# Kernel tuning notes

Hardware: AMD Instinct MI355X
Metric: run time of the kernel (lower is better)

The kernel has to match this reference:

```python
import jax, jax.numpy as jnp
import numpy as np

B, T, N, F_IN = 8, 24, 500, 64
FILT, GRU_H, HEADS = 128, 128, 8
CHEB, KMIX, EMB, TF, EF = 3, 8, 8, 32, 64
NS, WE = 20, 25


def setup_inputs():
    key = jax.random.key(0)
    ks = iter(jax.random.split(key, 80))
    def rn(shape, s=1.0):
        return jax.random.normal(next(ks), shape, dtype=jnp.float32) * s
    adj = jax.random.uniform(next(ks), (N, N), dtype=jnp.float32)
    adj = adj / adj.sum(axis=1, keepdims=True)  # row-normalized support, spectral radius ~1
    inp = dict(
        adj=adj,
        x=rn((B, T, F_IN, N)),
        grid_node_map=jax.random.uniform(next(ks), (NS * WE, N), dtype=jnp.float32),
        target_time=rn((B, 1, TF)),
        node_embed=rn((KMIX, N, EMB), 0.1),
        w_pool0=rn((EMB, CHEB, F_IN, FILT), 0.05), b_pool0=rn((EMB, FILT), 0.05),
        a0_f1w=rn((KMIX, F_IN), 0.1), a0_f1b=jnp.zeros(KMIX, jnp.float32),
        a0_f2w=rn((KMIX, KMIX), 0.1), a0_f2b=jnp.zeros(KMIX, jnp.float32),
        w_pool1=rn((EMB, CHEB, FILT, FILT), 0.05), b_pool1=rn((EMB, FILT), 0.05),
        a1_f1w=rn((KMIX, FILT), 0.1), a1_f1b=jnp.zeros(KMIX, jnp.float32),
        a1_f2w=rn((KMIX, KMIX), 0.1), a1_f2b=jnp.zeros(KMIX, jnp.float32),
        bn0_g=jnp.ones(FILT, jnp.float32), bn0_b=jnp.zeros(FILT, jnp.float32),
        bn1_g=jnp.ones(FILT, jnp.float32), bn1_b=jnp.zeros(FILT, jnp.float32),
        gru_wih=rn((3 * GRU_H, FILT), 0.05), gru_whh=rn((3 * GRU_H, GRU_H), 0.05),
        gru_bih=jnp.zeros(3 * GRU_H, jnp.float32), gru_bhh=jnp.zeros(3 * GRU_H, jnp.float32),
        bngru_g=jnp.ones(GRU_H, jnp.float32), bngru_b=jnp.zeros(GRU_H, jnp.float32),
        convq_w=rn((GRU_H, GRU_H, 1, 3), 0.05), convq_b=jnp.zeros(GRU_H, jnp.float32),
        convk_w=rn((GRU_H, GRU_H, 1, 3), 0.05), convk_b=jnp.zeros(GRU_H, jnp.float32),
        vw=rn((GRU_H, GRU_H), 0.05), vb=jnp.zeros(GRU_H, jnp.float32),
        ow=rn((GRU_H, GRU_H), 0.05), ob=jnp.zeros(GRU_H, jnp.float32),
        res1_w=rn((FILT, F_IN), 0.05), res1_b=jnp.zeros(FILT, jnp.float32),
        fc_w=rn((T,), 0.1), fc_b=jnp.zeros((1,), jnp.float32),
        resconv_w=rn((T,), 0.1), resconv_b=jnp.zeros((1,), jnp.float32),
        res2_w=rn((GRU_H, FILT), 0.05), res2_b=jnp.zeros(GRU_H, jnp.float32),
        bnres_g=jnp.ones(GRU_H, jnp.float32), bnres_b=jnp.zeros(GRU_H, jnp.float32),
        te1_w=rn((GRU_H, TF), 0.1), te1_b=jnp.zeros(GRU_H, jnp.float32),
        te2_w=rn((GRU_H, GRU_H), 0.05), te2_b=jnp.zeros(GRU_H, jnp.float32),
        fin_w=rn((EF, GRU_H), 0.05), fin_b=jnp.zeros(EF, jnp.float32),
    )
    return inp


def _bn(x, g, b, eps=1e-5):
    # training-mode batchnorm over all axes but channel-last (matches torch BN1d layouts used)
    axes = tuple(range(x.ndim - 1))
    m = x.mean(axes, keepdims=True)
    v = x.var(axes, keepdims=True)
    return (x - m) / jnp.sqrt(v + eps) * g + b


def _flexgcn(x, supports, node_pool, wp, bp, f1w, f1b, f2w, f2b):
    # x: [b, N, Cin]; supports: [K, N, N]; node_pool: [Kmix, N, E]
    pooled = x.mean(axis=1)  # adaptive avg pool over nodes -> [b, Cin]
    a = jax.nn.softmax(jax.nn.relu(pooled @ f1w.T + f1b) @ f2w.T + f2b, axis=-1)
    ne = jnp.einsum('bk,knd->bnd', a, node_pool)       # [b, N, E]
    xg = jnp.einsum('knm,bmc->bnkc', supports, x)      # [b, N, K, Cin]
    # fused form of einsum('bnd,dkio->bnkio') then ('bnki,bnkio->bno'):
    tmp = jnp.einsum('bnkc,dkco->bndo', xg, wp)        # [b, N, E, Cout]
    return jnp.einsum('bndo,bnd->bno', tmp, ne) + jnp.einsum('bnd,do->bno', ne, bp)


def reference(adj, x, grid_node_map, target_time, node_embed,
              w_pool0, b_pool0, a0_f1w, a0_f1b, a0_f2w, a0_f2b,
              w_pool1, b_pool1, a1_f1w, a1_f1b, a1_f2w, a1_f2b,
              bn0_g, bn0_b, bn1_g, bn1_b,
              gru_wih, gru_whh, gru_bih, gru_bhh, bngru_g, bngru_b,
              convq_w, convq_b, convk_w, convk_b, vw, vb, ow, ob,
              res1_w, res1_b, fc_w, fc_b, resconv_w, resconv_b,
              res2_w, res2_b, bnres_g, bnres_b,
              te1_w, te1_b, te2_w, te2_b, fin_w, fin_b):
    Bb, Tt, Dd, Nn = x.shape
    eye = jnp.eye(Nn, dtype=adj.dtype)
    supports = jnp.stack([eye, adj, 2.0 * adj @ adj - eye], axis=0)  # cheb_k = 3
    xr = x.reshape(Bb * Tt, Dd, Nn).transpose(0, 2, 1)  # [BT, N, D]
    res = xr
    out = _flexgcn(xr, supports, node_embed, w_pool0, b_pool0, a0_f1w, a0_f1b, a0_f2w, a0_f2b)
    out = jax.nn.relu(_bn(out, bn0_g, bn0_b))
    out = _flexgcn(out, supports, node_embed, w_pool1, b_pool1, a1_f1w, a1_f1b, a1_f2w, a1_f2b)
    out = jax.nn.relu(_bn(out, bn1_g, bn1_b))
    res = res @ res1_w.T + res1_b
    out2 = res + out                                    # [BT, N, FILT]
    res = out2
    # GRU over time per (batch, node)
    H = gru_whh.shape[1]
    seq = out2.reshape(Bb, Tt, Nn, -1).transpose(0, 2, 1, 3).reshape(Bb * Nn, Tt, -1)
    gi = seq @ gru_wih.T + gru_bih                      # [BN, T, 3H]
    def step(h, g):
        gh = h @ gru_whh.T + gru_bhh
        ir, iz, inn = jnp.split(g, 3, axis=-1)
        hr, hz, hn = jnp.split(gh, 3, axis=-1)
        r = jax.nn.sigmoid(ir + hr)
        z = jax.nn.sigmoid(iz + hz)
        n = jnp.tanh(inn + r * hn)
        h = (1.0 - z) * n + z * h
        return h, h
    _, hs = jax.lax.scan(step, jnp.zeros((Bb * Nn, H), seq.dtype), gi.transpose(1, 0, 2))
    out2 = hs.transpose(1, 0, 2).reshape(Bb, Nn, Tt, H)
    out2 = jax.nn.relu(_bn(out2, bngru_g, bngru_b))
    # temporal multi-head attention with conv-aware q/k
    h_ = HEADS
    dk = H // h_
    def conv_t(inp, w, b):
        y = jax.lax.conv_general_dilated(inp.transpose(0, 3, 1, 2), w, (1, 1), ((0, 0), (1, 1)))
        return y + b[None, :, None, None]               # [B, H, N, T]
    q = conv_t(out2, convq_w, convq_b).reshape(Bb, h_, dk, Nn, Tt).transpose(0, 3, 1, 4, 2)
    k = conv_t(out2, convk_w, convk_b).reshape(Bb, h_, dk, Nn, Tt).transpose(0, 3, 1, 4, 2)
    v = (out2 @ vw.T + vb).reshape(Bb, Nn, Tt, h_, dk).transpose(0, 1, 3, 2, 4)
    attn = jax.nn.softmax(jnp.einsum('bnhtd,bnhsd->bnhts', q, k) / (dk ** 0.5), axis=-1)
    xa = jnp.einsum('bnhts,bnhsd->bnhtd', attn, v).transpose(0, 1, 3, 2, 4).reshape(Bb, Nn, Tt, H)
    xa = xa @ ow.T + ob
    out2f = jnp.einsum('bntd,t->bnd', xa, fc_w) + fc_b  # Conv2d(seq_len -> 1, 1x1)
    res = (res @ res2_w.T + res2_b).reshape(Bb, Tt, Nn, -1)
    res = jnp.einsum('btnd,t->bnd', res, resconv_w) + resconv_b
    out2f = out2f + _bn(res, bnres_g, bnres_b)
    te = jax.nn.relu(target_time @ te1_w.T + te1_b) @ te2_w.T + te2_b  # [B, 1, H]
    out2f = (te + out2f) @ fin_w.T + fin_b              # [B, N, EF]
    g = jnp.einsum('gn,bne->bge', grid_node_map, out2f)
    return g.transpose(0, 2, 1).reshape(Bb, -1, NS, WE)
```

## Files before the change

### kernel.cpp

```cpp
#include <hip/hip_runtime.h>
#include <math.h>

using short8 = __attribute__((ext_vector_type(8))) short;
using f32x4  = __attribute__((ext_vector_type(4))) float;
using ushort_t = unsigned short;

__device__ __forceinline__ ushort_t f2b(float f){
  unsigned int u = __builtin_bit_cast(unsigned int, f);
  u = (u + 0x7fffu + ((u >> 16) & 1u)) >> 16;
  return (ushort_t)u;
}
__device__ __forceinline__ float b2f(ushort_t u){
  unsigned int v = ((unsigned int)u) << 16;
  return __builtin_bit_cast(float, v);
}
__device__ __forceinline__ uint2 pk4(float a, float b, float c, float d){
  uint2 p; p.x = (unsigned)f2b(a) | ((unsigned)f2b(b)<<16);
  p.y = (unsigned)f2b(c) | ((unsigned)f2b(d)<<16); return p;
}
__device__ __forceinline__ uint2 z2(){ return uint2{0u,0u}; }
__device__ __forceinline__ unsigned cvtpk(float lo, float hi){
  unsigned r; asm("v_cvt_pk_bf16_f32 %0, %1, %2" : "=v"(r) : "v"(lo), "v"(hi));
  return r;
}

__device__ __forceinline__ float fsig(float x){ return 1.f/(1.f+__expf(-x)); }
__device__ __forceinline__ float ftanh(float x){ return 1.f - 2.f/(1.f+__expf(2.f*x)); }
__device__ __forceinline__ void unp8(uint4 v, float* d){
  d[0]=b2f((ushort_t)(v.x&0xffffu)); d[1]=b2f((ushort_t)(v.x>>16));
  d[2]=b2f((ushort_t)(v.y&0xffffu)); d[3]=b2f((ushort_t)(v.y>>16));
  d[4]=b2f((ushort_t)(v.z&0xffffu)); d[5]=b2f((ushort_t)(v.z>>16));
  d[6]=b2f((ushort_t)(v.w&0xffffu)); d[7]=b2f((ushort_t)(v.w>>16));
}
__device__ __forceinline__ float4 unpk4f(uint2 v){
  float4 r;
  r.x = b2f((ushort_t)(v.x & 0xffffu)); r.y = b2f((ushort_t)(v.x >> 16));
  r.z = b2f((ushort_t)(v.y & 0xffffu)); r.w = b2f((ushort_t)(v.y >> 16));
  return r;
}

struct AgF32 { const float* A; int lda;
  __device__ uint2 load4p(int r, int k, int K) const {
    const float* p = &A[(size_t)r*lda + k];
    if (k+3 < K) { float4 v = *(const float4*)p; return pk4(v.x,v.y,v.z,v.w); }
    float a=0,b=0,c=0,d=0;
    if (k   < K) a = p[0];
    if (k+1 < K) b = p[1];
    if (k+2 < K) c = p[2];
    if (k+3 < K) d = p[3];
    return pk4(a,b,c,d); } };
struct AgBf16p { const ushort_t* A; int lda;
  __device__ uint2 load4p(int r, int k, int K) const {
    const ushort_t* p = &A[(size_t)r*lda + k];
    if (k+3 < K) return *(const uint2*)p;
    ushort_t a=0,b=0,c=0,d=0;
    if (k   < K) a = p[0];
    if (k+1 < K) b = p[1];
    if (k+2 < K) c = p[2];
    if (k+3 < K) d = p[3];
    uint2 q; q.x = (unsigned)a | ((unsigned)b<<16); q.y = (unsigned)c | ((unsigned)d<<16);
    return q; } };
struct AgStackA { const float* adj; const ushort_t* s2;
  __device__ uint2 load4p(int r, int k, int K) const {
    if (r < 500) {
      float a=0,b=0,c=0,d=0;
      const float* p = adj + (size_t)r*500 + k;
      if (k+3 < K) { float4 v = *(const float4*)p; return pk4(v.x,v.y,v.z,v.w); }
      if (k   < K) a = p[0];
      if (k+1 < K) b = p[1];
      if (k+2 < K) c = p[2];
      if (k+3 < K) d = p[3];
      return pk4(a,b,c,d);
    }
    const ushort_t* p = s2 + (size_t)(r-500)*500 + k;
    if (k+3 < K) return *(const uint2*)p;
    ushort_t a=0,b=0,c=0,d=0;
    if (k   < K) a = p[0];
    if (k+1 < K) b = p[1];
    if (k+2 < K) c = p[2];
    if (k+3 < K) d = p[3];
    uint2 q; q.x = (unsigned)a | ((unsigned)b<<16); q.y = (unsigned)c | ((unsigned)d<<16);
    return q; } };
struct AgXrow { const float* x;
  __device__ uint2 load4p(int r, int k, int K) const {
    int bt = r/500, n = r - bt*500;
    const float* p = x + (size_t)bt*32000 + n;
    float a=0,b=0,c=0,d=0;
    if (k   < K) a = p[(size_t)k*500];
    if (k+1 < K) b = p[(size_t)(k+1)*500];
    if (k+2 < K) c = p[(size_t)(k+2)*500];
    if (k+3 < K) d = p[(size_t)(k+3)*500];
    return pk4(a,b,c,d); } };
struct AgConvB { const ushort_t* hs;
  __device__ uint2 load4p(int r, int k, int) const {
    int t = r % 24; int dt = k >> 7; int c = k & 127; int t2 = t + dt - 1;
    if (t2 < 0 || t2 >= 24) return z2();
    return *(const uint2*)&hs[(size_t)(r + (t2 - t))*128 + c]; } };
struct AgTeAdd { const float* o2f; const float* te;
  __device__ uint2 load4p(int r, int k, int) const {
    float4 a = *(const float4*)&o2f[(size_t)r*128 + k];
    float4 b = *(const float4*)&te[(size_t)(r/500)*128 + k];
    return pk4(a.x+b.x, a.y+b.y, a.z+b.z, a.w+b.w); } };

struct BgPk { const ushort_t* B; int ldb;
  __device__ uint2 load4p(int c, int k, int K) const {
    const ushort_t* p = &B[(size_t)c*ldb + k];
    if (k+3 < K) return *(const uint2*)p;
    ushort_t a=0,b=0,cc=0,d=0;
    if (k   < K) a = p[0];
    if (k+1 < K) b = p[1];
    if (k+2 < K) cc = p[2];
    if (k+3 < K) d = p[3];
    uint2 q; q.x = (unsigned)a | ((unsigned)b<<16); q.y = (unsigned)cc | ((unsigned)d<<16);
    return q; } };
struct BgXTv { const float* x;
  __device__ uint2 load4p(int c, int k, int K) const {
    const float* p = x + (size_t)c*500 + k;
    if (k+3 < K) { float4 v = *(const float4*)p; return pk4(v.x,v.y,v.z,v.w); }
    float a=0,b=0,cc=0,d=0;
    if (k   < K) a = p[0];
    if (k+1 < K) b = p[1];
    if (k+2 < K) cc = p[2];
    if (k+3 < K) d = p[3];
    return pk4(a,b,cc,d); } };
struct BgAdjB { const float* adj;
  __device__ uint2 load4p(int c, int k, int K) const {
    float a=0,b=0,cc=0,d=0;
    if (k   < K) a = adj[(size_t)k*500 + c];
    if (k+1 < K) b = adj[(size_t)(k+1)*500 + c];
    if (k+2 < K) cc = adj[(size_t)(k+2)*500 + c];
    if (k+3 < K) d = adj[(size_t)(k+3)*500 + c];
    return pk4(a,b,cc,d); } };
struct BgY0T { const ushort_t* t;
  __device__ uint2 load4p(int c, int k, int K) const {
    const ushort_t* p = &t[((size_t)(c & 127)*192 + (c >> 7))*500 + k];
    if (k+3 < K) return *(const uint2*)p;
    ushort_t a=0,b=0,cc=0,d=0;
    if (k   < K) a = p[0];
    if (k+1 < K) b = p[1];
    if (k+2 < K) cc = p[2];
    if (k+3 < K) d = p[3];
    uint2 qq; qq.x = (unsigned)a | ((unsigned)b<<16); qq.y = (unsigned)cc | ((unsigned)d<<16);
    return qq; } };

struct EpNone { __device__ float operator()(int, int, float a) const { return a; } };
struct EpS2   { __device__ float operator()(int r, int c, float a) const { return 2.f*a - (r==c ? 1.f : 0.f); } };
struct EpBias { const float* b;
  __device__ float operator()(int, int c, float a) const { return a + b[c]; } };
struct EpRes1 { const ushort_t* out1; const float* st; const float *g, *bb, *rb; float invM;
  __device__ float operator()(int r, int c, float a) const {
    float mean = st[c]*invM; float var = st[128+c]*invM - mean*mean;
    float rstd = rsqrtf(var + 1e-5f);
    float y = (b2f(out1[(size_t)r*128 + c]) - mean)*rstd*g[c] + bb[c];
    y = fmaxf(y, 0.f);
    return a + rb[c] + y; } };
struct EpRes2 { const float *r2b, *rw, *rcb;
  __device__ float operator()(int, int c, float a) const {
    float s = 0.f;
    #pragma unroll
    for (int t=0; t<24; ++t) s += rw[t];
    return a + s*r2b[c] + rcb[0]; } };

template<int OMODE, class AG, class BG, class EP>
__global__ __launch_bounds__(256)
void gemm_mfma(AG ag, BG bg, EP ep, void* Cv, int M, int N, int K, int ldc) {
  constexpr int LDA = 40;
  __shared__ ushort_t As[128*LDA];
  __shared__ ushort_t Bs[128*LDA];
  int tid = threadIdx.x;
  int lane = tid & 63, wave = tid >> 6;
  int wr = (wave >> 1) * 64, wc = (wave & 1) * 64;
  int q = lane >> 4, r16 = lane & 15;
  int row0 = blockIdx.y*128, col0 = blockIdx.x*128;
  int am = tid >> 3, ak = (tid & 7) * 4;
  uint2 ua[4], ub[4];
  int nK = (K + 31) / 32;
  #pragma unroll
  for (int s=0;s<4;++s){
    int gr = row0 + am + 32*s;
    ua[s] = (gr < M) ? ag.load4p(gr, ak, K) : z2();
    int gc = col0 + am + 32*s;
    ub[s] = (gc < N) ? bg.load4p(gc, ak, K) : z2();
  }
  f32x4 acc[4][4] = {};
  for (int t=0; t<nK; ++t) {
    #pragma unroll
    for (int s=0;s<4;++s){
      *(uint2*)&As[(am + 32*s)*LDA + ak] = ua[s];
      *(uint2*)&Bs[(am + 32*s)*LDA + ak] = ub[s];
    }
    __syncthreads();
    if (t+1 < nK) {
      int k0 = (t+1)*32;
      #pragma unroll
      for (int s=0;s<4;++s){
        int gr = row0 + am + 32*s;
        ua[s] = (gr < M) ? ag.load4p(gr, k0+ak, K) : z2();
        int gc = col0 + am + 32*s;
        ub[s] = (gc < N) ? bg.load4p(gc, k0+ak, K) : z2();
      }
    }
    short8 a[4], b[4];
    #pragma unroll
    for (int it=0;it<4;++it) a[it] = *(const short8*)&As[(wr + it*16 + r16)*LDA + q*8];
    #pragma unroll
    for (int jt=0;jt<4;++jt) b[jt] = *(const short8*)&Bs[(wc + jt*16 + r16)*LDA + q*8];
    #pragma unroll
    for (int it=0;it<4;++it)
      #pragma unroll
      for (int jt=0;jt<4;++jt)
        acc[it][jt] = __builtin_amdgcn_mfma_f32_16x16x32_bf16(a[it], b[jt], acc[it][jt], 0, 0, 0);
    __syncthreads();
  }
  if constexpr (OMODE >= 2) {
    constexpr int CC = (OMODE == 2) ? 64 : 128;
    #pragma unroll
    for (int it=0;it<4;++it) {
      int rr0 = row0 + wr + it*16 + q*4;
      if (rr0 >= M) continue;
      int half = (rr0 >= 500) ? 1 : 0;
      int n0 = rr0 - half*500;
      #pragma unroll
      for (int jt=0;jt<4;++jt) {
        int c = col0 + wc + jt*16 + r16;
        if (c >= N) continue;
        int cin = c & (CC-1); int bt = c / CC;
        size_t addr = (size_t)(half*CC + cin)*96000 + (size_t)bt*500 + n0;
        *(uint2*)&((ushort_t*)Cv)[addr] =
            pk4(acc[it][jt][0], acc[it][jt][1], acc[it][jt][2], acc[it][jt][3]);
      }
    }
  } else {
    #pragma unroll
    for (int it=0;it<4;++it) {
      #pragma unroll
      for (int v=0;v<4;++v) {
        int rr = row0 + wr + it*16 + q*4 + v;
        if (rr >= M) continue;
        #pragma unroll
        for (int jt=0;jt<4;++jt) {
          int c = col0 + wc + jt*16 + r16;
          if (c >= N) continue;
          float val = ep(rr, c, acc[it][jt][v]);
          if (OMODE == 1) ((ushort_t*)Cv)[(size_t)rr*ldc + c] = f2b(val);
          else            ((float*)Cv)[(size_t)rr*ldc + c] = val;
        }
      }
    }
  }
}

template<bool XSRC, bool BOUT>
__global__ __launch_bounds__(256, 3)
void k_flex(const float* x, const ushort_t* xgT, const ushort_t* wpf,
            const float* ne, const float* bp, void* Cv, int nKC) {
  int tid = threadIdx.x;
  int lane = tid & 63, wave = tid >> 6;
  int wr = (wave >> 1) * 64, wc = (wave & 1) * 64;
  int q = lane >> 4, r16 = lane & 15;
  int row0 = blockIdx.x * 128;
  int rowIt[4]; size_t xoff[4];
  float ne8[4][8];
  #pragma unroll
  for (int it=0; it<4; ++it) {
    int r = row0 + wr + it*16 + r16;
    rowIt[it] = r;
    if (XSRC) { int bt = r/500; int n = r - bt*500; xoff[it] = (size_t)bt*32000 + n; }
    float4 p0 = *(const float4*)&ne[(size_t)r*8];
    float4 p1 = *(const float4*)&ne[(size_t)r*8 + 4];
    ne8[it][0]=p0.x; ne8[it][1]=p0.y; ne8[it][2]=p0.z; ne8[it][3]=p0.w;
    ne8[it][4]=p1.x; ne8[it][5]=p1.y; ne8[it][6]=p1.z; ne8[it][7]=p1.w;
  }
  int cB = wc + r16;
  f32x4 acc[4][4] = {};
  int nT = nKC >> 2;
  float vc[4]; uint4 bc[4];
  {
    int kc = q;
    #pragma unroll
    for (int jt=0;jt<4;++jt)
      bc[jt] = *(const uint4*)&wpf[((size_t)kc*128 + cB + jt*16)*8];
    #pragma unroll
    for (int it=0;it<4;++it) {
      if (XSRC) vc[it] = x[xoff[it] + (size_t)kc*500];
      else      vc[it] = b2f(xgT[(size_t)kc*96000 + rowIt[it]]);
    }
  }
  for (int t=0; t<nT; ++t) {
    float vn[4]; uint4 bnx[4];
    if (t+1 < nT) {
      int kc = (t+1)*4 + q;
      #pragma unroll
      for (int jt=0;jt<4;++jt)
        bnx[jt] = *(const uint4*)&wpf[((size_t)kc*128 + cB + jt*16)*8];
      bool fromX = XSRC && (kc < 64);
      if (fromX) {
        #pragma unroll
        for (int it=0;it<4;++it) vn[it] = x[xoff[it] + (size_t)kc*500];
      } else {
        int kcx = XSRC ? (kc - 64) : kc;
        #pragma unroll
        for (int it=0;it<4;++it) vn[it] = b2f(xgT[(size_t)kcx*96000 + rowIt[it]]);
      }
    } else {
      #pragma unroll
      for (int it=0;it<4;++it) vn[it] = 0.f;
      #pragma unroll
      for (int jt=0;jt<4;++jt) { bnx[jt].x=0u; bnx[jt].y=0u; bnx[jt].z=0u; bnx[jt].w=0u; }
    }
    short8 a[4], b[4];
    #pragma unroll
    for (int jt=0;jt<4;++jt) b[jt] = __builtin_bit_cast(short8, bc[jt]);
    #pragma unroll
    for (int it=0;it<4;++it) {
      float v = vc[it];
      uint4 pw;
      pw.x = cvtpk(v*ne8[it][0], v*ne8[it][1]);
      pw.y = cvtpk(v*ne8[it][2], v*ne8[it][3]);
      pw.z = cvtpk(v*ne8[it][4], v*ne8[it][5]);
      pw.w = cvtpk(v*ne8[it][6], v*ne8[it][7]);
      a[it] = __builtin_bit_cast(short8, pw);
    }
    #pragma unroll
    for (int it=0;it<4;++it)
      #pragma unroll
      for (int jt=0;jt<4;++jt)
        acc[it][jt] = __builtin_amdgcn_mfma_f32_16x16x32_bf16(a[it], b[jt], acc[it][jt], 0, 0, 0);
    #pragma unroll
    for (int it=0;it<4;++it) vc[it] = vn[it];
    #pragma unroll
    for (int jt=0;jt<4;++jt) bc[jt] = bnx[jt];
  }
  #pragma unroll
  for (int it=0;it<4;++it) {
    #pragma unroll
    for (int v=0;v<4;++v) {
      int rr = row0 + wr + it*16 + q*4 + v;
      #pragma unroll
      for (int jt=0;jt<4;++jt) {
        int c = wc + jt*16 + r16;
        float val = acc[it][jt][v];
        #pragma unroll
        for (int d=0; d<8; ++d) val += ne[(size_t)rr*8 + d]*bp[d*128 + c];
        if (BOUT) ((ushort_t*)Cv)[(size_t)rr*128 + c] = f2b(val);
        else      ((float*)Cv)[(size_t)rr*128 + c] = val;
      }
    }
  }
}

__global__ void k_pack_bf(const float* s, ushort_t* d, int n){
  int i = blockIdx.x*256 + threadIdx.x; if (i < n) d[i] = f2b(s[i]); }
__global__ void k_pack_wpf(const float* wp, ushort_t* d, int C, int KC){
  int i = blockIdx.x*256 + threadIdx.x; int total = KC*128*8; if (i >= total) return;
  int e = i & 7; int rest = i >> 3; int c = rest & 127; int kc = rest >> 7;
  int kk = kc / C; int cin = kc - kk*C;
  d[i] = f2b(wp[(((size_t)e*3 + kk)*C + cin)*128 + c]); }
__global__ void k_pack_qkvw(const float* cqw, const float* ckw, const float* vw, ushort_t* d){
  int i = blockIdx.x*256 + threadIdx.x; if (i >= 147456) return;
  int o = i / 384; int r = i - o*384; int dt = r >> 7; int cin = r & 127;
  float v;
  if (o < 128) v = cqw[((size_t)o*128 + cin)*3 + dt];
  else if (o < 256) v = ckw[((size_t)(o-128)*128 + cin)*3 + dt];
  else v = (dt==1) ? vw[(size_t)(o-256)*128 + cin] : 0.f;
  d[i] = f2b(v); }
__global__ void k_pack_qkvb(const float* cqb, const float* ckb, const float* vb, float* d){
  int i = threadIdx.x;
  d[i] = (i<128) ? cqb[i] : (i<256) ? ckb[i-128] : vb[i-256]; }

__global__ void k_fuseB(const float* out0, const float* st, const float* g, const float* b,
                        ushort_t* y0t, float* pooled) {
  __shared__ float tile[32][33];
  __shared__ float red[8][32];
  int bt = blockIdx.z; int n0 = blockIdx.x*32; int o0 = blockIdx.y*32;
  int tx = threadIdx.x, ty = threadIdx.y;
  int o = o0 + tx;
  float mean = st[o]*(1.f/96000.f);
  float var  = st[128+o]*(1.f/96000.f) - mean*mean;
  float sc = rsqrtf(var + 1e-5f)*g[o];
  float bb = b[o] - mean*sc;
  float psum = 0.f;
  for (int i = ty; i < 32; i += 8) {
    int n = n0 + i;
    float y = 0.f;
    if (n < 500) {
      float v = out0[((size_t)bt*500 + n)*128 + o];
      y = fmaxf(v*sc + bb, 0.f);
      psum += y;
    }
    tile[i][tx] = y;
  }
  red[ty][tx] = psum;
  __syncthreads();
  if (ty == 0) {
    float s = red[0][tx];
    #pragma unroll
    for (int k=1;k<8;++k) s += red[k][tx];
    atomicAdd(&pooled[bt*128 + o], s*(1.f/500.f));
  }
  for (int i = ty; i < 32; i += 8) {
    int oo = o0 + i; int n = n0 + tx;
    if (n < 500) y0t[(size_t)oo*96000 + (size_t)bt*500 + n] = f2b(tile[tx][i]);
  }
}

__global__ void k_pool0(const float* x, float* pooled) {
  int bt = blockIdx.x; int c = threadIdx.x;
  const float* p = x + (size_t)bt*32000 + (size_t)c*500;
  float s = 0.f;
  for (int n=0;n<500;++n) s += p[n];
  pooled[bt*64 + c] = s*(1.f/500.f);
}

__global__ __launch_bounds__(128) void k_mlp_p(const float* pooled, int F,
                      const float* f1w, const float* f1b,
                      const float* f2w, const float* f2b, float* aout) {
  int bt = blockIdx.x; int c = threadIdx.x;
  __shared__ float red2[2][8];
  __shared__ float hsh[8];
  float p = (c < F) ? pooled[bt*F + c] : 0.f;
  #pragma unroll
  for (int k=0;k<8;++k){
    float v = (c < F) ? p*f1w[k*F + c] : 0.f;
    #pragma unroll
    for (int off=32; off>0; off>>=1) v += __shfl_down(v, off);
    if ((c & 63) == 0) red2[c>>6][k] = v;
  }
  __syncthreads();
  if (c < 8) {
    float s = red2[0][c] + red2[1][c] + f1b[c];
    hsh[c] = fmaxf(s, 0.f);
  }
  __syncthreads();
  if (c == 0) {
    float z[8]; float m = -1e30f;
    #pragma unroll
    for (int k2=0;k2<8;++k2){
      float s = f2b[k2];
      #pragma unroll
      for (int k=0;k<8;++k) s += hsh[k]*f2w[k2*8 + k];
      z[k2] = s; m = fmaxf(m, s);
    }
    float den = 0.f;
    #pragma unroll
    for (int k2=0;k2<8;++k2){ z[k2] = __expf(z[k2]-m); den += z[k2]; }
    float inv = 1.f/den;
    #pragma unroll
    for (int k2=0;k2<8;++k2) aout[bt*8 + k2] = z[k2]*inv;
  }
}

__global__ void k_ne(const float* a, const float* emb, float* ne) {
  int i = blockIdx.x*256 + threadIdx.x;
  if (i >= 768000) return;
  int d = i & 7; int rem = i >> 3; int n = rem % 500; int bt = rem / 500;
  float s = 0.f;
  #pragma unroll
  for (int k=0;k<8;++k) s += a[bt*8 + k]*emb[((size_t)k*500 + n)*8 + d];
  ne[i] = s;
}

__global__ void k_bn_stats(const float* src, float* stats, int M, int rpb) {
  int col = threadIdx.x & 127; int seg = threadIdx.x >> 7;
  int r0 = blockIdx.x * rpb; int r1 = r0 + rpb; if (r1 > M) r1 = M;
  float s = 0.f, q = 0.f;
  for (int r = r0 + seg; r < r1; r += 2) {
    float v = src[(size_t)r*128 + col];
    s += v; q += v*v;
  }
  atomicAdd(&stats[col], s);
  atomicAdd(&stats[128+col], q);
}
__global__ void k_bn_stats_bf(const ushort_t* src, float* stats, int M, int rpb) {
  int col = threadIdx.x & 127; int seg = threadIdx.x >> 7;
  int r0 = blockIdx.x * rpb; int r1 = r0 + rpb; if (r1 > M) r1 = M;
  float s = 0.f, q = 0.f;
  for (int r = r0 + seg; r < r1; r += 2) {
    float v = b2f(src[(size_t)r*128 + col]);
    s += v; q += v*v;
  }
  atomicAdd(&stats[col], s);
  atomicAdd(&stats[128+col], q);
}

__global__ void k_bn_apply4(float* dst, const float* src, const float* st,
                            const float* g, const float* b, int total4, float invM, int relu, int addd) {
  int i = blockIdx.x*256 + threadIdx.x;
  if (i >= total4) return;
  int i4 = i*4; int c = i4 & 127;
  float4 sm = *(const float4*)&st[c];
  float4 sq = *(const float4*)&st[128+c];
  float4 g4 = *(const float4*)&g[c];
  float4 b4 = *(const float4*)&b[c];
  float4 v = *(const float4*)&src[i4];
  float4 y;
  {
    float mean = sm.x*invM; float var = sq.x*invM - mean*mean;
    y.x = (v.x-mean)*rsqrtf(var+1e-5f)*g4.x + b4.x;
    mean = sm.y*invM; var = sq.y*invM - mean*mean;
    y.y = (v.y-mean)*rsqrtf(var+1e-5f)*g4.y + b4.y;
    mean = sm.z*invM; var = sq.z*invM - mean*mean;
    y.z = (v.z-mean)*rsqrtf(var+1e-5f)*g4.z + b4.z;
    mean = sm.w*invM; var = sq.w*invM - mean*mean;
    y.w = (v.w-mean)*rsqrtf(var+1e-5f)*g4.w + b4.w;
  }
  if (relu){ y.x=fmaxf(y.x,0.f); y.y=fmaxf(y.y,0.f); y.z=fmaxf(y.z,0.f); y.w=fmaxf(y.w,0.f); }
  if (addd){ float4 d0 = *(const float4*)&dst[i4]; y.x+=d0.x; y.y+=d0.y; y.z+=d0.z; y.w+=d0.w; }
  *(float4*)&dst[i4] = y;
}

__global__ void k_bn_apply_bf_ip(ushort_t* buf, const float* st,
                                 const float* g, const float* b, int total4, float invM) {
  int i = blockIdx.x*256 + threadIdx.x;
  if (i >= total4) return;
  int i4 = i*4; int c = i4 & 127;
  uint2 vv = *(const uint2*)&buf[i4];
  float v0 = b2f((ushort_t)(vv.x & 0xffffu)), v1 = b2f((ushort_t)(vv.x >> 16));
  float v2 = b2f((ushort_t)(vv.y & 0xffffu)), v3 = b2f((ushort_t)(vv.y >> 16));
  float4 sm = *(const float4*)&st[c];
  float4 sq = *(const float4*)&st[128+c];
  float4 g4 = *(const float4*)&g[c];
  float4 b4 = *(const float4*)&b[c];
  float mean, var, y0, y1, y2, y3;
  mean = sm.x*invM; var = sq.x*invM - mean*mean;
  y0 = (v0-mean)*rsqrtf(var+1e-5f)*g4.x + b4.x;
  mean = sm.y*invM; var = sq.y*invM - mean*mean;
  y1 = (v1-mean)*rsqrtf(var+1e-5f)*g4.y + b4.y;
  mean = sm.z*invM; var = sq.z*invM - mean*mean;
  y2 = (v2-mean)*rsqrtf(var+1e-5f)*g4.z + b4.z;
  mean = sm.w*invM; var = sq.w*invM - mean*mean;
  y3 = (v3-mean)*rsqrtf(var+1e-5f)*g4.w + b4.w;
  y0=fmaxf(y0,0.f); y1=fmaxf(y1,0.f); y2=fmaxf(y2,0.f); y3=fmaxf(y3,0.f);
  *(uint2*)&buf[i4] = pk4(y0,y1,y2,y3);
}

__global__ __launch_bounds__(256, 1) void k_gru_mfma(
    const ushort_t* gi, const ushort_t* whhp, const float* bhh,
    ushort_t* hsb, float* stats) {
  __shared__ ushort_t hbf[16*128];
  __shared__ float    uh[16*384];

  int tid  = threadIdx.x;
  int lane = tid & 63;
  int wave = tid >> 6;
  int r16  = lane & 15, q = lane >> 4;

  short8 bfrag[6][4];
  #pragma unroll
  for (int j=0;j<6;++j){
    int col = (wave*6 + j)*16 + r16;
    #pragma unroll
    for (int kk=0;kk<4;++kk)
      bfrag[j][kk] = *(const short8*)&whhp[(size_t)col*128 + kk*32 + q*8];
  }

  int gr = tid >> 4;
  int gc = tid & 15;
  int u0 = gc*8;
  int s  = blockIdx.x*16 + gr;
  int b  = s / 500, n = s - b*500;
  size_t gi_base = ((size_t)b*24*500 + n)*384;
  size_t hs_base = (size_t)s*24*128 + u0;

  float bh0[8], bh1[8], bh2[8];
  #pragma unroll
  for (int k=0;k<8;++k){ bh0[k]=bhh[u0+k]; bh1[k]=bhh[128+u0+k]; bh2[k]=bhh[256+u0+k]; }

  float h[8], sacc[8], qacc[8];
  #pragma unroll
  for (int k=0;k<8;++k){ h[k]=0.f; sacc[k]=0.f; qacc[k]=0.f; }
  {
    int phys = gr*128 + ((gc ^ (gr&7))*8);
    uint4 zz; zz.x=0u; zz.y=0u; zz.z=0u; zz.w=0u;
    *(uint4*)&hbf[phys] = zz;
  }

  for (int t=0;t<24;++t){
    __syncthreads();
    const ushort_t* gp = gi + gi_base + (size_t)t*192000;
    uint4 gir = *(const uint4*)&gp[u0];
    uint4 giz = *(const uint4*)&gp[128+u0];
    uint4 gin = *(const uint4*)&gp[256+u0];

    short8 afrag[4];
    #pragma unroll
    for (int kk=0;kk<4;++kk)
      afrag[kk] = *(const short8*)&hbf[r16*128 + (((kk<<2)+q) ^ (r16&7))*8];
    #pragma unroll
    for (int j=0;j<6;++j){
      f32x4 acc = {};
      #pragma unroll
      for (int kk=0;kk<4;++kk)
        acc = __builtin_amdgcn_mfma_f32_16x16x32_bf16(afrag[kk], bfrag[j][kk], acc, 0, 0, 0);
      int col = (wave*6+j)*16 + r16;
      #pragma unroll
      for (int v=0;v<4;++v){
        int rr = q*4 + v;
        uh[rr*384 + ((((col>>2) ^ (rr&7))<<2) | (col&3))] = acc[v];
      }
    }
    __syncthreads();

    float hr[8], hz[8], hn[8];
    {
      int rw = gr*384; int sw = gr & 7;
      int c0 = (u0>>2);
      float4 A, Bv;
      A  = *(const float4*)&uh[rw + ((c0      ^ sw)<<2)];
      Bv = *(const float4*)&uh[rw + (((c0+1)  ^ sw)<<2)];
      hr[0]=A.x; hr[1]=A.y; hr[2]=A.z; hr[3]=A.w; hr[4]=Bv.x; hr[5]=Bv.y; hr[6]=Bv.z; hr[7]=Bv.w;
      int c1 = ((128+u0)>>2);
      A  = *(const float4*)&uh[rw + ((c1      ^ sw)<<2)];
      Bv = *(const float4*)&uh[rw + (((c1+1)  ^ sw)<<2)];
      hz[0]=A.x; hz[1]=A.y; hz[2]=A.z; hz[3]=A.w; hz[4]=Bv.x; hz[5]=Bv.y; hz[6]=Bv.z; hz[7]=Bv.w;
      int c2 = ((256+u0)>>2);
      A  = *(const float4*)&uh[rw + ((c2      ^ sw)<<2)];
      Bv = *(const float4*)&uh[rw + (((c2+1)  ^ sw)<<2)];
      hn[0]=A.x; hn[1]=A.y; hn[2]=A.z; hn[3]=A.w; hn[4]=Bv.x; hn[5]=Bv.y; hn[6]=Bv.z; hn[7]=Bv.w;
    }
    float ir[8], iz[8], in_[8];
    unp8(gir, ir); unp8(giz, iz); unp8(gin, in_);
    #pragma unroll
    for (int k=0;k<8;++k){
      float rg = fsig(ir[k] + hr[k] + bh0[k]);
      float zg = fsig(iz[k] + hz[k] + bh1[k]);
      float ng = ftanh(in_[k] + rg*(hn[k] + bh2[k]));
      float hv = (1.f - zg)*ng + zg*h[k];
      h[k] = hv;
      sacc[k] += hv; qacc[k] += hv*hv;
    }
    uint2 p0 = pk4(h[0],h[1],h[2],h[3]);
    uint2 p1 = pk4(h[4],h[5],h[6],h[7]);
    uint4 pw; pw.x=p0.x; pw.y=p0.y; pw.z=p1.x; pw.w=p1.y;
    {
      int phys = gr*128 + ((gc ^ (gr&7))*8);
      *(uint4*)&hbf[phys] = pw;
    }
    *(uint4*)&hsb[hs_base + (size_t)t*128] = pw;
  }

  __syncthreads();
  #pragma unroll
  for (int k=0;k<8;++k) uh[gr*128 + u0 + k] = sacc[k];
  __syncthreads();
  if (tid < 128) {
    float ss = 0.f;
    for (int r=0;r<16;++r) ss += uh[r*128 + tid];
    atomicAdd(&stats[tid], ss);
  }
  __syncthreads();
  #pragma unroll
  for (int k=0;k<8;++k) uh[gr*128 + u0 + k] = qacc[k];
  __syncthreads();
  if (tid < 128) {
    float qq = 0.f;
    for (int r=0;r<16;++r) qq += uh[r*128 + tid];
    atomicAdd(&stats[128 + tid], qq);
  }
}

__global__ __launch_bounds__(256) void k_attn3(const ushort_t* QKV,
    const float* ow, const float* ob, const float* fcw, const float* fcb, float* out2f) {
  __shared__ float A1[24*128];
  __shared__ float A2[24*128];
  __shared__ float Sc[8][24][25];
  __shared__ float red[256];
  int bn = blockIdx.x; int tid = threadIdx.x;
  size_t base = (size_t)bn*9216;
  for (int i=tid;i<768;i+=256){
    int t=i>>5, c4=i&31;
    uint2 q2 = *(const uint2*)&QKV[base + (size_t)t*384 + c4*4];
    uint2 k2 = *(const uint2*)&QKV[base + (size_t)t*384 + 128 + c4*4];
    int phys = t*128 + ((c4^(t&7))<<2);
    *(float4*)&A1[phys] = unpk4f(q2);
    *(float4*)&A2[phys] = unpk4f(k2);
  }
  __syncthreads();
  for (int i=tid;i<4608;i+=256){
    int hh = i/576; int r = i - hh*576; int t = r/24; int s_ = r - t*24;
    float d0 = 0.f, d1 = 0.f;
    #pragma unroll
    for (int dd4=0;dd4<4;++dd4){
      float4 qv = *(const float4*)&A1[t*128 + ((((hh<<2)+dd4)^(t&7))<<2)];
      float4 kv = *(const float4*)&A2[s_*128 + ((((hh<<2)+dd4)^(s_&7))<<2)];
      d0 += qv.x*kv.x + qv.y*kv.y;
      d1 += qv.z*kv.z + qv.w*kv.w;
    }
    Sc[hh][t][s_] = (d0+d1)*0.25f;
  }
  __syncthreads();
  for (int i=tid;i<768;i+=256){
    int t=i>>5, c4=i&31;
    uint2 v2 = *(const uint2*)&QKV[base + (size_t)t*384 + 256 + c4*4];
    *(float4*)&A2[t*128 + ((c4^(t&7))<<2)] = unpk4f(v2);
  }
  if (tid < 192) {
    int hh = tid/24, t = tid - (tid/24)*24;
    float m = -1e30f;
    for (int s_=0;s_<24;++s_) m = fmaxf(m, Sc[hh][t][s_]);
    float den = 0.f;
    for (int s_=0;s_<24;++s_){ float e = __expf(Sc[hh][t][s_]-m); Sc[hh][t][s_] = e; den += e; }
    float inv = 1.f/den;
    for (int s_=0;s_<24;++s_) Sc[hh][t][s_] *= inv;
  }
  __syncthreads();
  for (int i=tid;i<768;i+=256){
    int t = i>>5; int o4 = i&31; int hh = o4>>2;
    float4 s = {0.f,0.f,0.f,0.f};
    #pragma unroll
    for (int s_=0;s_<24;++s_){
      float p = Sc[hh][t][s_];
      float4 v = *(const float4*)&A2[s_*128 + ((o4^(s_&7))<<2)];
      s.x += p*v.x; s.y += p*v.y; s.z += p*v.z; s.w += p*v.w;
    }
    *(float4*)&A1[t*128 + ((o4^(t&7))<<2)] = s;
  }
  __syncthreads();
  int o = tid & 127, hf = tid >> 7;
  {
    float s = 0.f;
    for (int t = hf*12; t < hf*12 + 12; ++t)
      s += fcw[t]*A1[t*128 + ((((o>>2)^(t&7))<<2) | (o&3))];
    red[tid] = s;
  }
  __syncthreads();
  float* xbar = &Sc[0][0][0];
  if (tid < 128) xbar[tid] = red[tid] + red[tid+128];
  __syncthreads();
  {
    float s = 0.f;
    for (int c = hf*64; c < hf*64 + 64; ++c) s += xbar[c]*ow[o*128 + c];
    red[tid] = s;
  }
  __syncthreads();
  if (tid < 128) {
    float sfc = 0.f;
    for (int t=0;t<24;++t) sfc += fcw[t];
    out2f[(size_t)bn*128 + o] = red[tid] + red[tid+128] + sfc*ob[o] + fcb[0];
  }
}

__global__ void k_rbar_bf(const ushort_t* out2, const float* rw, float* rbar) {
  int i = blockIdx.x*256 + threadIdx.x;
  if (i >= 512000) return;
  int c = i & 127; int bnn = i >> 7; int b = bnn/500, n = bnn - b*500;
  float s = 0.f;
  #pragma unroll
  for (int t=0;t<24;++t) s += rw[t] * b2f(out2[((size_t)(b*24 + t)*500 + n)*128 + c]);
  rbar[i] = s;
}

__global__ void k_te(const float* tt, const float* w1, const float* b1,
                     const float* w2, const float* b2, float* te) {
  __shared__ float h1[128];
  int b = blockIdx.x; int o = threadIdx.x;
  float s = b1[o];
  for (int c=0;c<32;++c) s += tt[b*32 + c]*w1[o*32 + c];
  h1[o] = fmaxf(s, 0.f);
  __syncthreads();
  float s2 = b2[o];
  for (int c=0;c<128;++c) s2 += h1[c]*w2[o*128 + c];
  te[b*128 + o] = s2;
}

__global__ void k_grid(const float* gnm, const float* fin, float* out) {
  int e = threadIdx.x & 63; int gq = threadIdx.x >> 6;
  int g = blockIdx.x*4 + gq; int b = blockIdx.y;
  float s = 0.f;
  const float* gr = gnm + (size_t)g*500;
  const float* fb = fin + (size_t)b*500*64 + e;
  for (int n=0;n<500;++n) s += gr[n] * fb[(size_t)n*64];
  out[(size_t)b*32000 + (size_t)e*500 + g] = s;
}

extern "C" void kernel_launch(void* const* d_in, const int* in_sizes, int n_in,
                              void* d_out, int out_size, void* d_ws, size_t ws_size,
                              hipStream_t stream) {
  const float* adj   = (const float*)d_in[0];
  const float* x     = (const float*)d_in[1];
  const float* gnm   = (const float*)d_in[2];
  const float* ttime = (const float*)d_in[3];
  const float* emb   = (const float*)d_in[4];
  const float* wp0   = (const float*)d_in[5];
  const float* bp0   = (const float*)d_in[6];
  const float* a0f1w = (const float*)d_in[7];
  const float* a0f1b = (const float*)d_in[8];
  const float* a0f2w = (const float*)d_in[9];
  const float* a0f2b = (const float*)d_in[10];
  const float* wp1   = (const float*)d_in[11];
  const float* bp1   = (const float*)d_in[12];
  const float* a1f1w = (const float*)d_in[13];
  const float* a1f1b = (const float*)d_in[14];
  const float* a1f2w = (const float*)d_in[15];
  const float* a1f2b = (const float*)d_in[16];
  const float* bn0g  = (const float*)d_in[17];
  const float* bn0b  = (const float*)d_in[18];
  const float* bn1g  = (const float*)d_in[19];
  const float* bn1b  = (const float*)d_in[20];
  const float* wih   = (const float*)d_in[21];
  const float* whh   = (const float*)d_in[22];
  const float* bih   = (const float*)d_in[23];
  const float* bhh   = (const float*)d_in[24];
  const float* bgg   = (const float*)d_in[25];
  const float* bgb   = (const float*)d_in[26];
  const float* cqw   = (const float*)d_in[27];
  const float* cqb   = (const float*)d_in[28];
  const float* ckw   = (const float*)d_in[29];
  const float* ckb   = (const float*)d_in[30];
  const float* vw    = (const float*)d_in[31];
  const float* vb    = (const float*)d_in[32];
  const float* ow    = (const float*)d_in[33];
  const float* ob    = (const float*)d_in[34];
  const float* r1w   = (const float*)d_in[35];
  const float* r1b   = (const float*)d_in[36];
  const float* fcw   = (const float*)d_in[37];
  const float* fcb   = (const float*)d_in[38];
  const float* rcw   = (const float*)d_in[39];
  const float* rcb   = (const float*)d_in[40];
  const float* r2w   = (const float*)d_in[41];
  const float* r2b   = (const float*)d_in[42];
  const float* bnrg  = (const float*)d_in[43];
  const float* bnrb  = (const float*)d_in[44];
  const float* te1w  = (const float*)d_in[45];
  const float* te1b  = (const float*)d_in[46];
  const float* te2w  = (const float*)d_in[47];
  const float* te2b  = (const float*)d_in[48];
  const float* finw  = (const float*)d_in[49];
  const float* finb  = (const float*)d_in[50];
  float* dout = (float*)d_out;
  float* W = (float*)d_ws;

  size_t off = 0;
  auto alloc = [&](size_t n){ size_t r = off; off += (n + 255) & ~(size_t)255; return r; };
  size_t oStats = alloc(512);
  size_t oPool  = alloc(24576);
  size_t oAmix  = alloc(1536);
  size_t oTe    = alloc(1024);
  size_t oO2f   = alloc(512000);
  size_t oRbar  = alloc(512000);
  size_t oRes   = alloc(512000);
  size_t oFin   = alloc(256000);
  size_t oNe0   = alloc(768000);
  size_t oNe1   = alloc(768000);
  size_t oS2    = alloc(125000);
  size_t oWpf0  = alloc(98304);
  size_t oWpf1  = alloc(196608);
  size_t oR1wp  = alloc(4096);
  size_t oWihp  = alloc(24576);
  size_t oWhhp  = alloc(24576);
  size_t oQkvw  = alloc(73728);
  size_t oQkvb  = alloc(384);
  size_t oR2wp  = alloc(8192);
  size_t oFinwp = alloc(4096);
  size_t oR1    = alloc(12288000);
  size_t oR2    = alloc(12288000);
  size_t oR4    = alloc(6144000);
  size_t oOut1  = alloc(6144000);
  (void)n_in; (void)in_sizes; (void)out_size;
  if (ws_size < off * sizeof(float)) return;

  float* stats = W + oStats;
  float* pooled= W + oPool;
  float* amix  = W + oAmix;
  float* teb   = W + oTe;
  float* out2f = W + oO2f;
  float* rbar  = W + oRbar;
  float* resout= W + oRes;
  float* fin   = W + oFin;
  float* ne0   = W + oNe0;
  float* ne1   = W + oNe1;
  ushort_t* S2bf  = (ushort_t*)(W + oS2);
  ushort_t* wpf0  = (ushort_t*)(W + oWpf0);
  ushort_t* wpf1  = (ushort_t*)(W + oWpf1);
  ushort_t* r1wp  = (ushort_t*)(W + oR1wp);
  ushort_t* wihp  = (ushort_t*)(W + oWihp);
  ushort_t* whhp  = (ushort_t*)(W + oWhhp);
  ushort_t* qkvwp = (ushort_t*)(W + oQkvw);
  float*    qkvb  = W + oQkvb;
  ushort_t* r2wp  = (ushort_t*)(W + oR2wp);
  ushort_t* finwp = (ushort_t*)(W + oFinwp);
  float* out0  = W + oR1;
  ushort_t* out2b = (ushort_t*)(W + oR1);
  ushort_t* xgT1 = (ushort_t*)(W + oR2);
  ushort_t* gi16 = (ushort_t*)(W + oR2);
  ushort_t* qkv16= (ushort_t*)(W + oR2);
  ushort_t* xgT0 = (ushort_t*)(W + oR4);
  ushort_t* out1 = (ushort_t*)(W + oOut1);
  ushort_t* hsb  = (ushort_t*)(W + oOut1);

  k_pack_wpf<<<768, 256, 0, stream>>>(wp0, wpf0, 64, 192);
  k_pack_wpf<<<1536, 256, 0, stream>>>(wp1, wpf1, 128, 384);
  k_pack_bf<<<32, 256, 0, stream>>>(r1w, r1wp, 8192);
  k_pack_bf<<<192, 256, 0, stream>>>(wih, wihp, 49152);
  k_pack_bf<<<192, 256, 0, stream>>>(whh, whhp, 49152);
  k_pack_bf<<<64, 256, 0, stream>>>(r2w, r2wp, 16384);
  k_pack_bf<<<32, 256, 0, stream>>>(finw, finwp, 8192);
  k_pack_qkvw<<<576, 256, 0, stream>>>(cqw, ckw, vw, qkvwp);
  k_pack_qkvb<<<1, 384, 0, stream>>>(cqb, ckb, vb, qkvb);

  gemm_mfma<1><<<dim3(4,4), 256, 0, stream>>>(
      AgF32{adj,500}, BgAdjB{adj}, EpS2{}, (void*)S2bf, 500, 500, 500, 500);
  gemm_mfma<2><<<dim3(96,8), 256, 0, stream>>>(
      AgStackA{adj, S2bf}, BgXTv{x}, EpNone{}, (void*)xgT0, 1000, 12288, 500, 0);
  k_pool0<<<192, 64, 0, stream>>>(x, pooled);
  k_mlp_p<<<192, 128, 0, stream>>>(pooled, 64, a0f1w, a0f1b, a0f2w, a0f2b, amix);
  k_ne<<<3000, 256, 0, stream>>>(amix, emb, ne0);
  k_flex<true, false><<<750, 256, 0, stream>>>(
      x, xgT0, wpf0, ne0, bp0, (void*)out0, 192);
  hipMemsetAsync((void*)stats, 0, 256*sizeof(float), stream);
  k_bn_stats<<<768, 256, 0, stream>>>(out0, stats, 96000, 125);

  hipMemsetAsync((void*)pooled, 0, 24576*sizeof(float), stream);
  k_fuseB<<<dim3(16,4,192), dim3(32,8), 0, stream>>>(out0, stats, bn0g, bn0b, xgT1, pooled);
  k_mlp_p<<<192, 128, 0, stream>>>(pooled, 128, a1f1w, a1f1b, a1f2w, a1f2b, amix);
  k_ne<<<3000, 256, 0, stream>>>(amix, emb, ne1);
  gemm_mfma<3><<<dim3(192,8), 256, 0, stream>>>(
      AgStackA{adj, S2bf}, BgY0T{xgT1}, EpNone{},
      (void*)(xgT1 + (size_t)128*96000), 1000, 24576, 500, 0);
  k_flex<false, true><<<750, 256, 0, stream>>>(
      x, xgT1, wpf1, ne1, bp1, (void*)out1, 384);
  hipMemsetAsync((void*)stats, 0, 256*sizeof(float), stream);
  k_bn_stats_bf<<<768, 256, 0, stream>>>(out1, stats, 96000, 125);
  gemm_mfma<1><<<dim3(1,750), 256, 0, stream>>>(
      AgXrow{x}, BgPk{r1wp,64}, EpRes1{out1, stats, bn1g, bn1b, r1b, 1.f/96000.f},
      (void*)out2b, 96000, 128, 64, 128);

  k_rbar_bf<<<2000, 256, 0, stream>>>(out2b, rcw, rbar);
  gemm_mfma<0><<<dim3(1,32), 256, 0, stream>>>(
      AgF32{rbar,128}, BgPk{r2wp,128}, EpRes2{r2b, rcw, rcb}, (void*)resout, 4000, 128, 128, 128);
  hipMemsetAsync((void*)stats, 0, 256*sizeof(float), stream);
  k_bn_stats<<<32, 256, 0, stream>>>(resout, stats, 4000, 125);

  gemm_mfma<1><<<dim3(3,750), 256, 0, stream>>>(
      AgBf16p{out2b,128}, BgPk{wihp,128}, EpBias{bih}, (void*)gi16, 96000, 384, 128, 384);
  hipMemsetAsync((void*)(stats+256), 0, 256*sizeof(float), stream);
  k_gru_mfma<<<250, 256, 0, stream>>>(gi16, whhp, bhh, hsb, stats+256);
  k_bn_apply_bf_ip<<<12000, 256, 0, stream>>>(hsb, stats+256, bgg, bgb, 3072000, 1.f/96000.f);

  gemm_mfma<1><<<dim3(3,750), 256, 0, stream>>>(
      AgConvB{hsb}, BgPk{qkvwp,384}, EpBias{qkvb}, (void*)qkv16, 96000, 384, 384, 384);
  k_attn3<<<4000, 256, 0, stream>>>(qkv16, ow, ob, fcw, fcb, out2f);

  k_bn_apply4<<<500, 256, 0, stream>>>(out2f, resout, stats, bnrg, bnrb, 128000, 1.f/4000.f, 0, 1);
  k_te<<<8, 128, 0, stream>>>(ttime, te1w, te1b, te2w, te2b, teb);
  gemm_mfma<0><<<dim3(1,32), 256, 0, stream>>>(
      AgTeAdd{out2f, teb}, BgPk{finwp,128}, EpBias{finb}, (void*)fin, 4000, 64, 128, 64);
  k_grid<<<dim3(125,8), 256, 0, stream>>>(gnm, fin, dout);
}
```

Baseline: 1.135 ms.

## Reshape k_flex wave tiling to 32x128 per wave and drop B-fragment prefetch

Each wave in k_flex now covers 32 rows by all 128 output columns instead of a 64x64 quadrant. The per-row A-fragment construction (scaling by node embeddings and converting to bf16) is therefore done for 2 row tiles instead of 4, so each wave does less VALU conversion work. In exchange every wave loads all 8 weight fragments per k-step. The register double-buffering of weight fragments is removed, so those loads are issued in-loop with less latency hiding.

```diff
diff --git a/kernel.cpp b/kernel.cpp
--- a/kernel.cpp
+++ b/kernel.cpp
@@ -256,13 +256,13 @@
             const float* ne, const float* bp, void* Cv, int nKC) {
   int tid = threadIdx.x;
   int lane = tid & 63, wave = tid >> 6;
-  int wr = (wave >> 1) * 64, wc = (wave & 1) * 64;
   int q = lane >> 4, r16 = lane & 15;
+  int wr = wave * 32;
   int row0 = blockIdx.x * 128;
-  int rowIt[4]; size_t xoff[4];
-  float ne8[4][8];
-  #pragma unroll
-  for (int it=0; it<4; ++it) {
+  int rowIt[2]; size_t xoff[2];
+  float ne8[2][8];
+  #pragma unroll
+  for (int it=0; it<2; ++it) {
     int r = row0 + wr + it*16 + r16;
     rowIt[it] = r;
     if (XSRC) { int bt = r/500; int n = r - bt*500; xoff[it] = (size_t)bt*32000 + n; }
@@ -271,48 +271,41 @@
     ne8[it][0]=p0.x; ne8[it][1]=p0.y; ne8[it][2]=p0.z; ne8[it][3]=p0.w;
     ne8[it][4]=p1.x; ne8[it][5]=p1.y; ne8[it][6]=p1.z; ne8[it][7]=p1.w;
   }
-  int cB = wc + r16;
-  f32x4 acc[4][4] = {};
+  f32x4 acc[2][8] = {};
   int nT = nKC >> 2;
-  float vc[4]; uint4 bc[4];
+  float vc[2];
   {
     int kc = q;
     #pragma unroll
-    for (int jt=0;jt<4;++jt)
-      bc[jt] = *(const uint4*)&wpf[((size_t)kc*128 + cB + jt*16)*8];
-    #pragma unroll
-    for (int it=0;it<4;++it) {
+    for (int it=0;it<2;++it) {
       if (XSRC) vc[it] = x[xoff[it] + (size_t)kc*500];
       else      vc[it] = b2f(xgT[(size_t)kc*96000 + rowIt[it]]);
     }
   }
   for (int t=0; t<nT; ++t) {
-    float vn[4]; uint4 bnx[4];
+    int kc = t*4 + q;
+    uint4 bc[8];
+    #pragma unroll
+    for (int jt=0;jt<8;++jt)
+      bc[jt] = *(const uint4*)&wpf[((size_t)kc*128 + jt*16 + r16)*8];
+    float vn[2];
     if (t+1 < nT) {
-      int kc = (t+1)*4 + q;
-      #pragma unroll
-      for (int jt=0;jt<4;++jt)
-        bnx[jt] = *(const uint4*)&wpf[((size_t)kc*128 + cB + jt*16)*8];
-      bool fromX = XSRC && (kc < 64);
+      int kcn = (t+1)*4 + q;
+      bool fromX = XSRC && (kcn < 64);
       if (fromX) {
         #pragma unroll
-        for (int it=0;it<4;++it) vn[it] = x[xoff[it] + (size_t)kc*500];
+        for (int it=0;it<2;++it) vn[it] = x[xoff[it] + (size_t)kcn*500];
       } else {
-        int kcx = XSRC ? (kc - 64) : kc;
+        int kcx = XSRC ? (kcn - 64) : kcn;
         #pragma unroll
-        for (int it=0;it<4;++it) vn[it] = b2f(xgT[(size_t)kcx*96000 + rowIt[it]]);
+        for (int it=0;it<2;++it) vn[it] = b2f(xgT[(size_t)kcx*96000 + rowIt[it]]);
       }
-    } else {
-      #pragma unroll
-      for (int it=0;it<4;++it) vn[it] = 0.f;
-      #pragma unroll
-      for (int jt=0;jt<4;++jt) { bnx[jt].x=0u; bnx[jt].y=0u; bnx[jt].z=0u; bnx[jt].w=0u; }
-    }
-    short8 a[4], b[4];
-    #pragma unroll
-    for (int jt=0;jt<4;++jt) b[jt] = __builtin_bit_cast(short8, bc[jt]);
-    #pragma unroll
-    for (int it=0;it<4;++it) {
+    } else { vn[0]=0.f; vn[1]=0.f; }
+    short8 a[2], b[8];
+    #pragma unroll
+    for (int jt=0;jt<8;++jt) b[jt] = __builtin_bit_cast(short8, bc[jt]);
+    #pragma unroll
+    for (int it=0;it<2;++it) {
       float v = vc[it];
       uint4 pw;
       pw.x = cvtpk(v*ne8[it][0], v*ne8[it][1]);
@@ -322,23 +315,20 @@
       a[it] = __builtin_bit_cast(short8, pw);
     }
     #pragma unroll
-    for (int it=0;it<4;++it)
+    for (int it=0;it<2;++it)
       #pragma unroll
-      for (int jt=0;jt<4;++jt)
+      for (int jt=0;jt<8;++jt)
         acc[it][jt] = __builtin_amdgcn_mfma_f32_16x16x32_bf16(a[it], b[jt], acc[it][jt], 0, 0, 0);
-    #pragma unroll
-    for (int it=0;it<4;++it) vc[it] = vn[it];
-    #pragma unroll
-    for (int jt=0;jt<4;++jt) bc[jt] = bnx[jt];
-  }
-  #pragma unroll
-  for (int it=0;it<4;++it) {
+    vc[0]=vn[0]; vc[1]=vn[1];
+  }
+  #pragma unroll
+  for (int it=0;it<2;++it) {
     #pragma unroll
     for (int v=0;v<4;++v) {
       int rr = row0 + wr + it*16 + q*4 + v;
       #pragma unroll
-      for (int jt=0;jt<4;++jt) {
-        int c = wc + jt*16 + r16;
+      for (int jt=0;jt<8;++jt) {
+        int c = jt*16 + r16;
         float val = acc[it][jt][v];
         #pragma unroll
         for (int d=0; d<8; ++d) val += ne[(size_t)rr*8 + d]*bp[d*128 + c];
```

New measurement: 1.143 ms. No clear change (+0.7%).
